# Performance work log

Measured on AMD Instinct MI355X. Metric: run time of the kernel, lower is better.

Reference implementation:

```python
import jax, jax.numpy as jnp
import numpy as np

MARGIN = 0.1
PERM_SEED = 42  # fixed stand-in for torch.randperm per row


def setup_inputs() -> dict:
    key = jax.random.key(0)
    k1, k2, k3 = jax.random.split(key, 3)
    n, d, f = 32768, 1000, 300
    inputs = jax.random.normal(k1, (n, f), dtype=jnp.float32)
    Y = jax.random.normal(k2, (d, f), dtype=jnp.float32)
    y_idxs = jax.random.randint(k3, (n,), 0, d)
    return {"inputs": inputs, "Y": Y, "y_idxs": y_idxs}


def reference(inputs, Y, y_idxs):
    # inputs: [n, f], Y: [d, f] class semantic embeddings, y_idxs: [n]
    n, d = inputs.shape[0], Y.shape[0]

    # All dot products at once: S[i, j] = Y[j] . inputs[i]
    S = inputs @ Y.T  # [n, d]

    # One random class permutation per row (torch.randperm(d) per sample)
    perm_keys = jax.random.split(jax.random.key(PERM_SEED), n)
    perms = jax.vmap(lambda k: jax.random.permutation(k, d))(perm_keys)  # [n, d]

    ap = S[jnp.arange(n), y_idxs]                 # [n]   anchor-positive dots
    an = jnp.take_along_axis(S, perms, axis=1)    # [n, d] anchor-negative dots in perm order

    valid = perms != y_idxs[:, None]              # skip j == y
    # early-break condition at each permutation slot
    cond = valid & ((ap[:, None] - an) > MARGIN)
    c = cond.astype(jnp.int32)
    excl_cum = jnp.cumsum(c, axis=1) - c          # exclusive cumsum of break events
    # include every valid slot up to AND including the first breaking slot
    include = valid & (excl_cum == 0)             # [n, d]

    # MarginRankingLoss with target=1: mean(max(0, margin + an - ap))
    per_pair = jnp.maximum(0.0, MARGIN + an - ap[:, None])
    total = jnp.sum(jnp.where(include, per_pair, 0.0))
    count = jnp.maximum(jnp.sum(include), 1).astype(jnp.float32)
    return total / count
```

## Files before the change

### kernel.cpp

```cpp
#include <hip/hip_runtime.h>
#include <stdint.h>

#define N_ROWS 32768
#define D_CLS  1000
#define D_PAD  1024
#define F_DIM  300
#define F_PAD  320
#define MARGIN 0.1f

#define BM     128
#define BN     128
#define BK     64
#define GTHR   512
#define LDTA   328
#define LDTB   72

#define M_PB   32
#define NTHR   512
#define NT_PW  8
#define MT_PB  2
#define LDA    328
#define SROW   34

#define NPART  32

typedef short short8 __attribute__((ext_vector_type(8)));
typedef float f32x4  __attribute__((ext_vector_type(4)));

__device__ __forceinline__ uint32_t rotl32(uint32_t x, int r) {
  return (x << r) | (x >> (32 - r));
}

__device__ __forceinline__ void threefry2x32(uint32_t k0, uint32_t k1,
                                             uint32_t x0, uint32_t x1,
                                             uint32_t& o0, uint32_t& o1) {
  uint32_t k2 = k0 ^ k1 ^ 0x1BD11BDAu;
  x0 += k0; x1 += k1;
#define TF_R(r) { x0 += x1; x1 = rotl32(x1, (r)); x1 ^= x0; }
  TF_R(13) TF_R(15) TF_R(26) TF_R(6)
  x0 += k1; x1 += k2 + 1u;
  TF_R(17) TF_R(29) TF_R(16) TF_R(24)
  x0 += k2; x1 += k0 + 2u;
  TF_R(13) TF_R(15) TF_R(26) TF_R(6)
  x0 += k0; x1 += k1 + 3u;
  TF_R(17) TF_R(29) TF_R(16) TF_R(24)
  x0 += k1; x1 += k2 + 4u;
  TF_R(13) TF_R(15) TF_R(26) TF_R(6)
  x0 += k2; x1 += k0 + 5u;
#undef TF_R
  o0 = x0; o1 = x1;
}

struct TFSched {
  uint32_t k0, k1, k2, k2p1, k0p2, k1p3, k2p4, k0p5;
};
__device__ __forceinline__ TFSched tf_make(uint32_t k0, uint32_t k1) {
  TFSched s;
  s.k0 = k0; s.k1 = k1;
  s.k2 = k0 ^ k1 ^ 0x1BD11BDAu;
  s.k2p1 = s.k2 + 1u; s.k0p2 = k0 + 2u; s.k1p3 = k1 + 3u;
  s.k2p4 = s.k2 + 4u; s.k0p5 = k0 + 5u;
  return s;
}
__device__ __forceinline__ uint32_t tf_hash(const TFSched& s, uint32_t c) {
  uint32_t x0 = s.k0, x1 = c + s.k1;
#define TFH(r) { x0 += x1; x1 = __builtin_amdgcn_alignbit(x1, x1, 32 - (r)); x1 ^= x0; }
  TFH(13) TFH(15) TFH(26) TFH(6)
  x0 += s.k1; x1 += s.k2p1;
  TFH(17) TFH(29) TFH(16) TFH(24)
  x0 += s.k2; x1 += s.k0p2;
  TFH(13) TFH(15) TFH(26) TFH(6)
  x0 += s.k0; x1 += s.k1p3;
  TFH(17) TFH(29) TFH(16) TFH(24)
  x0 += s.k1; x1 += s.k2p4;
  TFH(13) TFH(15) TFH(26) TFH(6)
  x0 += s.k2; x1 += s.k0p5;
#undef TFH
  return x0 ^ x1;
}

__device__ __forceinline__ uint16_t f2bf(float f) {
  uint32_t u = __builtin_bit_cast(uint32_t, f);
  return (uint16_t)((u + 0x7FFFu + ((u >> 16) & 1u)) >> 16);
}
__device__ __forceinline__ float bf2f(uint16_t v) {
  return __builtin_bit_cast(float, (uint32_t)v << 16);
}
__device__ __forceinline__ float bf2f_lo(uint32_t v) {
  return __builtin_bit_cast(float, v << 16);
}
__device__ __forceinline__ float bf2f_hi(uint32_t v) {
  return __builtin_bit_cast(float, v & 0xFFFF0000u);
}

__global__ void prep(const float* __restrict__ Y, uint16_t* __restrict__ Ybf,
                     uint32_t* __restrict__ subk) {
  int i = blockIdx.x * 256 + threadIdx.x;
  if (i < D_PAD * F_PAD) {
    int j = i / F_PAD;
    int k = i - j * F_PAD;
    float v = (j < D_CLS && k < F_DIM) ? Y[j * F_DIM + k] : 0.f;
    Ybf[i] = f2bf(v);
  }
  if (i < N_ROWS) {
    uint32_t r1, r2, s1, s2;
    threefry2x32(0u, 42u, 0u, (uint32_t)i, r1, r2);
    threefry2x32(r1, r2, 0u, 1u, s1, s2);
    subk[2 * i]     = s1;
    subk[2 * i + 1] = s2;
  }
}

__launch_bounds__(GTHR, 1)
__global__ void gemm_s(const float* __restrict__ inputs,
                       const uint16_t* __restrict__ Ybf,
                       uint32_t* __restrict__ Spair) {
  __shared__ __align__(16) uint16_t A_lds[BM * LDTA];
  __shared__ __align__(16) uint16_t B_lds[2][BN * LDTB];

  const int t    = threadIdx.x;
  const int wave = t >> 6;
  const int lane = t & 63;
  const int l15  = lane & 15;
  const int g    = lane >> 4;
  const int wm   = wave >> 1;
  const int wn   = wave & 1;
  const int r0   = blockIdx.x * BM;

  for (int i = t; i < BM * (F_DIM / 4); i += GTHR) {
    int r  = i / 75;
    int c4 = i - r * 75;
    float4 v = *(const float4*)(inputs + (size_t)(r0 + r) * F_DIM + c4 * 4);
    ushort4 o;
    o.x = f2bf(v.x); o.y = f2bf(v.y); o.z = f2bf(v.z); o.w = f2bf(v.w);
    *(ushort4*)&A_lds[r * LDTA + c4 * 4] = o;
  }
  for (int i = t; i < BM * 7; i += GTHR) {
    int r = i / 7, p = i - r * 7;
    *(ushort4*)&A_lds[r * LDTA + 300 + p * 4] = (ushort4){0, 0, 0, 0};
  }

  const int brow = t >> 3, bkof = t & 7;
  short8 bv[2];
  auto LOADB = [&](int tile) {
    const int c0 = (tile / 5) * BN;
    const int k0 = (tile % 5) * BK;
#pragma unroll
    for (int j = 0; j < 2; ++j)
      bv[j] = *(const short8*)(Ybf + (size_t)(c0 + j * 64 + brow) * F_PAD + k0 + bkof * 8);
  };
  auto WRITEB = [&](int buf) {
#pragma unroll
    for (int j = 0; j < 2; ++j)
      *(short8*)&B_lds[buf][(j * 64 + brow) * LDTB + bkof * 8] = bv[j];
  };

  f32x4 acc[2][4];
#pragma unroll
  for (int mt = 0; mt < 2; ++mt)
#pragma unroll
    for (int nt = 0; nt < 4; ++nt) acc[mt][nt] = (f32x4){0.f, 0.f, 0.f, 0.f};

  LOADB(0);
  __syncthreads();
  WRITEB(0);
  __syncthreads();

  const int NT = 8 * 5;
#pragma unroll 1
  for (int tile = 0; tile < NT; ++tile) {
    const int kt = tile % 5;
    if (tile < NT - 1) LOADB(tile + 1);
    const uint16_t* Bc = B_lds[tile & 1];
#pragma unroll
    for (int ks = 0; ks < 2; ++ks) {
      short8 a[2], b[4];
#pragma unroll
      for (int mt = 0; mt < 2; ++mt)
        a[mt] = *(const short8*)&A_lds[(wm * 32 + mt * 16 + l15) * LDTA + kt * BK + ks * 32 + g * 8];
#pragma unroll
      for (int nt = 0; nt < 4; ++nt)
        b[nt] = *(const short8*)&Bc[(wn * 64 + nt * 16 + l15) * LDTB + ks * 32 + g * 8];
#pragma unroll
      for (int mt = 0; mt < 2; ++mt)
#pragma unroll
        for (int nt = 0; nt < 4; ++nt)
          acc[mt][nt] = __builtin_amdgcn_mfma_f32_16x16x32_bf16(a[mt], b[nt], acc[mt][nt], 0, 0, 0);
    }
    if (kt == 4) {
      const int c0 = (tile / 5) * BN;
#pragma unroll
      for (int mt = 0; mt < 2; ++mt)
#pragma unroll
        for (int nt = 0; nt < 4; ++nt) {
          const int col = c0 + wn * 64 + nt * 16 + l15;
#pragma unroll
          for (int p = 0; p < 2; ++p) {
            uint32_t lo = f2bf(acc[mt][nt][2 * p]);
            uint32_t hi = f2bf(acc[mt][nt][2 * p + 1]);
            size_t rp = (size_t)(r0 >> 1) + wm * 16 + mt * 8 + g * 2 + p;
            Spair[rp * D_PAD + col] = (hi << 16) | lo;
          }
          acc[mt][nt] = (f32x4){0.f, 0.f, 0.f, 0.f};
        }
    }
    if (tile < NT - 1) {
      WRITEB((tile + 1) & 1);
      __syncthreads();
    }
  }
}

__launch_bounds__(256, 2)
__global__ void hash_loss(const uint32_t* __restrict__ Spair,
                          const uint32_t* __restrict__ subk,
                          const int* __restrict__ yidx,
                          float* __restrict__ rowSum,
                          int* __restrict__ rowCnt) {
  const int lane = threadIdx.x & 63;
  const int wave = threadIdx.x >> 6;
  const int rp   = blockIdx.x * 4 + wave;
  const int rA   = 2 * rp;
  const int rB   = 2 * rp + 1;

  const int yA = yidx[rA], yB = yidx[rB];
  const TFSched sA = tf_make(subk[2 * rA], subk[2 * rA + 1]);
  const TFSched sB = tf_make(subk[2 * rB], subk[2 * rB + 1]);

  const uint32_t* Sp = Spair + (size_t)rp * D_PAD;
  const float apA = bf2f_lo(Sp[yA]);
  const float apB = bf2f_hi(Sp[yB]);

  uint32_t an[16];
#pragma unroll
  for (int j = 0; j < 4; ++j) {
    uint4 v = *(const uint4*)(Sp + j * 256 + lane * 4);
    an[4 * j + 0] = v.x; an[4 * j + 1] = v.y;
    an[4 * j + 2] = v.z; an[4 * j + 3] = v.w;
  }

  uint32_t skAB[16];
  uint32_t pkA = 0xFFFFFFFFu, pkB = 0xFFFFFFFFu;
#pragma unroll
  for (int q = 0; q < 16; ++q) {
    const int c = (q >> 2) * 256 + lane * 4 + (q & 3);
    uint32_t kA = tf_hash(sA, (uint32_t)c);
    uint32_t kB = tf_hash(sB, (uint32_t)c);
    skAB[q] = (kA >> 16) | (kB & 0xFFFF0000u);
    float anA = bf2f_lo(an[q]);
    float anB = bf2f_hi(an[q]);
    if ((c < D_CLS) && (c != yA) && (apA - anA) > MARGIN) {
      pkA = (kA < pkA) ? kA : pkA;
    }
    if ((c < D_CLS) && (c != yB) && (apB - anB) > MARGIN) {
      pkB = (kB < pkB) ? kB : pkB;
    }
  }
#pragma unroll
  for (int off = 1; off < 64; off <<= 1) {
    uint32_t oA = __shfl_xor(pkA, off, 64);
    uint32_t oB = __shfl_xor(pkB, off, 64);
    pkA = (oA < pkA) ? oA : pkA;
    pkB = (oB < pkB) ? oB : pkB;
  }
  const uint32_t pA16 = pkA >> 16;
  const uint32_t pB16 = pkB >> 16;

  float smA = 0.f, smB = 0.f; int ctA = 0, ctB = 0;
#pragma unroll
  for (int q = 0; q < 16; ++q) {
    const int c = (q >> 2) * 256 + lane * 4 + (q & 3);
    float anA = bf2f_lo(an[q]);
    float anB = bf2f_hi(an[q]);
    if ((c < D_CLS) && (c != yA) && (skAB[q] & 0xFFFFu) < pA16) {
      smA += MARGIN + anA - apA; ctA += 1;
    }
    if ((c < D_CLS) && (c != yB) && (skAB[q] >> 16) < pB16) {
      smB += MARGIN + anB - apB; ctB += 1;
    }
  }
#pragma unroll
  for (int off = 1; off < 64; off <<= 1) {
    smA += __shfl_xor(smA, off, 64);
    smB += __shfl_xor(smB, off, 64);
    ctA += __shfl_xor(ctA, off, 64);
    ctB += __shfl_xor(ctB, off, 64);
  }
  if (lane == 0) {
    rowSum[rA] = smA;
    rowCnt[rA] = ctA + (pkA != 0xFFFFFFFFu ? 1 : 0);
    rowSum[rB] = smB;
    rowCnt[rB] = ctB + (pkB != 0xFFFFFFFFu ? 1 : 0);
  }
}

__launch_bounds__(NTHR, 4)
__global__ void triplet_fused(const float* __restrict__ inputs,
                              const uint16_t* __restrict__ Ybf,
                              const int* __restrict__ yidx,
                              float* __restrict__ rowSum,
                              int* __restrict__ rowCnt) {
  __shared__ __align__(16) uint16_t SH[D_PAD * SROW];
  __shared__ int      y_sh[M_PB];
  __shared__ uint32_t subk_sh[M_PB][2];

  const int t    = threadIdx.x;
  const int wave = t >> 6;
  const int lane = t & 63;
  const int l15  = lane & 15;
  const int g    = lane >> 4;
  const int row0 = blockIdx.x * M_PB;
  const int colbase = wave * (NT_PW * 16);

  if (t < M_PB) {
    y_sh[t] = yidx[row0 + t];
    uint32_t r1, r2, s1, s2;
    threefry2x32(0u, 42u, 0u, (uint32_t)(row0 + t), r1, r2);
    threefry2x32(r1, r2, 0u, 1u, s1, s2);
    subk_sh[t][0] = s1; subk_sh[t][1] = s2;
  }

  uint16_t* A_fl = SH;
  for (int i = t; i < M_PB * (F_DIM / 4); i += NTHR) {
    int r  = i / 75;
    int c4 = i - r * 75;
    float4 v = *(const float4*)(inputs + (size_t)(row0 + r) * F_DIM + c4 * 4);
    ushort4 o;
    o.x = f2bf(v.x); o.y = f2bf(v.y); o.z = f2bf(v.z); o.w = f2bf(v.w);
    *(ushort4*)&A_fl[r * LDA + c4 * 4] = o;
  }
  for (int i = t; i < M_PB * 5; i += NTHR) {
    int r = i / 5, p = i - r * 5;
    *(ushort4*)&A_fl[r * LDA + 300 + p * 4] = (ushort4){0, 0, 0, 0};
  }
  __syncthreads();

  f32x4 acc[MT_PB][NT_PW];
#pragma unroll
  for (int mt = 0; mt < MT_PB; ++mt)
#pragma unroll
    for (int nt = 0; nt < NT_PW; ++nt) acc[mt][nt] = (f32x4){0.f, 0.f, 0.f, 0.f};

  const uint16_t* gB[NT_PW];
#pragma unroll
  for (int nt = 0; nt < NT_PW; ++nt) {
    int j = colbase + nt * 16 + l15;
    gB[nt] = Ybf + (size_t)j * F_PAD + (g << 3);
  }
  const uint16_t* aBase = &A_fl[l15 * LDA + (g << 3)];

#pragma unroll 2
  for (int ks = 0; ks < F_PAD / 32; ++ks) {
    short8 b[NT_PW], a[MT_PB];
#pragma unroll
    for (int nt = 0; nt < NT_PW; ++nt)
      b[nt] = *(const short8*)(gB[nt] + ks * 32);
#pragma unroll
    for (int mt = 0; mt < MT_PB; ++mt)
      a[mt] = *(const short8*)(aBase + mt * 16 * LDA + ks * 32);
#pragma unroll
    for (int mt = 0; mt < MT_PB; ++mt)
#pragma unroll
      for (int nt = 0; nt < NT_PW; ++nt)
        acc[mt][nt] = __builtin_amdgcn_mfma_f32_16x16x32_bf16(a[mt], b[nt], acc[mt][nt], 0, 0, 0);
  }

  __syncthreads();

#pragma unroll
  for (int mt = 0; mt < MT_PB; ++mt)
#pragma unroll
    for (int nt = 0; nt < NT_PW; ++nt) {
      int col = colbase + nt * 16 + l15;
#pragma unroll
      for (int p = 0; p < 2; ++p) {
        uint32_t lo = f2bf(acc[mt][nt][2 * p]);
        uint32_t hi = f2bf(acc[mt][nt][2 * p + 1]);
        *(uint32_t*)&SH[col * SROW + mt * 16 + (g << 2) + 2 * p] = (hi << 16) | lo;
      }
    }
  __syncthreads();

#pragma unroll
  for (int pr = 0; pr < 2; ++pr) {
    const int rA = wave * 4 + pr * 2;
    const int rB = rA + 1;
    const int yA = y_sh[rA], yB = y_sh[rB];
    const uint32_t a1 = subk_sh[rA][0], a2 = subk_sh[rA][1];
    const uint32_t b1 = subk_sh[rB][0], b2 = subk_sh[rB][1];
    const float apA = bf2f(SH[yA * SROW + rA]);
    const float apB = bf2f(SH[yB * SROW + rB]);

    uint32_t skA[16], skB[16];
    uint32_t pkA = 0xFFFFFFFFu, pkB = 0xFFFFFFFFu;
#pragma unroll
    for (int q = 0; q < 16; ++q) {
      const int c = q * 64 + lane;
      uint32_t xA, yAo, xB, yBo;
      threefry2x32(a1, a2, 0u, (uint32_t)c, xA, yAo);
      threefry2x32(b1, b2, 0u, (uint32_t)c, xB, yBo);
      skA[q] = xA ^ yAo;
      skB[q] = xB ^ yBo;
      float anA = bf2f(SH[c * SROW + rA]);
      float anB = bf2f(SH[c * SROW + rB]);
      if ((c < D_CLS) && (c != yA) && (apA - anA) > MARGIN) {
        pkA = (skA[q] < pkA) ? skA[q] : pkA;
      }
      if ((c < D_CLS) && (c != yB) && (apB - anB) > MARGIN) {
        pkB = (skB[q] < pkB) ? skB[q] : pkB;
      }
    }
#pragma unroll
    for (int off = 1; off < 64; off <<= 1) {
      uint32_t oA = __shfl_xor(pkA, off, 64);
      uint32_t oB = __shfl_xor(pkB, off, 64);
      pkA = (oA < pkA) ? oA : pkA;
      pkB = (oB < pkB) ? oB : pkB;
    }
    float smA = 0.f, smB = 0.f; int ctA = 0, ctB = 0;
#pragma unroll
    for (int q = 0; q < 16; ++q) {
      const int c = q * 64 + lane;
      float anA = bf2f(SH[c * SROW + rA]);
      float anB = bf2f(SH[c * SROW + rB]);
      if ((c < D_CLS) && (c != yA) && skA[q] < pkA) { smA += MARGIN + anA - apA; ctA += 1; }
      if ((c < D_CLS) && (c != yB) && skB[q] < pkB) { smB += MARGIN + anB - apB; ctB += 1; }
    }
#pragma unroll
    for (int off = 1; off < 64; off <<= 1) {
      smA += __shfl_xor(smA, off, 64);
      smB += __shfl_xor(smB, off, 64);
      ctA += __shfl_xor(ctA, off, 64);
      ctB += __shfl_xor(ctB, off, 64);
    }
    if (lane == 0) {
      rowSum[row0 + rA] = smA;
      rowCnt[row0 + rA] = ctA + (pkA != 0xFFFFFFFFu ? 1 : 0);
      rowSum[row0 + rB] = smB;
      rowCnt[row0 + rB] = ctB + (pkB != 0xFFFFFFFFu ? 1 : 0);
    }
  }
}

__global__ void reduce_part(const float* __restrict__ rowSum,
                            const int* __restrict__ rowCnt,
                            float* __restrict__ pS, int* __restrict__ pC) {
  __shared__ float ss[4];
  __shared__ int   sc[4];
  const int base = blockIdx.x * (N_ROWS / NPART);
  float s = 0.f; int c = 0;
  for (int i = threadIdx.x; i < N_ROWS / NPART; i += 256) {
    s += rowSum[base + i];
    c += rowCnt[base + i];
  }
#pragma unroll
  for (int off = 32; off > 0; off >>= 1) {
    s += __shfl_down(s, (unsigned)off, 64);
    c += __shfl_down(c, (unsigned)off, 64);
  }
  int wid = threadIdx.x >> 6, lane = threadIdx.x & 63;
  if (lane == 0) { ss[wid] = s; sc[wid] = c; }
  __syncthreads();
  if (threadIdx.x == 0) {
    pS[blockIdx.x] = ss[0] + ss[1] + ss[2] + ss[3];
    pC[blockIdx.x] = sc[0] + sc[1] + sc[2] + sc[3];
  }
}

__global__ void reduce_final(const float* __restrict__ pS,
                             const int* __restrict__ pC,
                             float* __restrict__ out) {
  const int lane = threadIdx.x;
  float s = (lane < NPART) ? pS[lane] : 0.f;
  int   c = (lane < NPART) ? pC[lane] : 0;
#pragma unroll
  for (int off = 32; off > 0; off >>= 1) {
    s += __shfl_down(s, (unsigned)off, 64);
    c += __shfl_down(c, (unsigned)off, 64);
  }
  if (lane == 0) out[0] = s / (float)(c < 1 ? 1 : c);
}

extern "C" void kernel_launch(void* const* d_in, const int* in_sizes, int n_in,
                              void* d_out, int out_size, void* d_ws, size_t ws_size,
                              hipStream_t stream) {
  const float* inputs = (const float*)d_in[0];
  const float* Y      = (const float*)d_in[1];
  const int*   yidx   = (const int*)d_in[2];
  float* out = (float*)d_out;

  char* ws = (char*)d_ws;
  size_t off = 0;
  uint16_t* Ybf    = (uint16_t*)(ws + off); off += (size_t)D_PAD * F_PAD * 2;
  float*    rowSum = (float*)(ws + off);    off += (size_t)N_ROWS * 4;
  int*      rowCnt = (int*)(ws + off);      off += (size_t)N_ROWS * 4;
  uint32_t* subk   = (uint32_t*)(ws + off); off += (size_t)N_ROWS * 8;
  float*    pS     = (float*)(ws + off);    off += (size_t)NPART * 4;
  int*      pC     = (int*)(ws + off);      off += (size_t)NPART * 4;
  off = (off + 255) & ~(size_t)255;
  uint32_t* Spair  = (uint32_t*)(ws + off); off += (size_t)(N_ROWS / 2) * D_PAD * 4;
  const size_t need = off;

  hipLaunchKernelGGL(prep, dim3((D_PAD * F_PAD + 255) / 256), dim3(256),
                     0, stream, Y, Ybf, subk);
  if (ws_size >= need) {
    hipLaunchKernelGGL(gemm_s, dim3(N_ROWS / BM), dim3(GTHR),
                       0, stream, inputs, Ybf, Spair);
    hipLaunchKernelGGL(hash_loss, dim3(N_ROWS / 8), dim3(256),
                       0, stream, Spair, subk, yidx, rowSum, rowCnt);
  } else {
    hipLaunchKernelGGL(triplet_fused, dim3(N_ROWS / M_PB), dim3(NTHR),
                       0, stream, inputs, Ybf, yidx, rowSum, rowCnt);
  }
  hipLaunchKernelGGL(reduce_part, dim3(NPART), dim3(256), 0, stream,
                     rowSum, rowCnt, pS, pC);
  hipLaunchKernelGGL(reduce_final, dim3(1), dim3(64), 0, stream, pS, pC, out);
}
```

Before: 122.6 us.

## Fuse permutation hashing and loss epilogue into the GEMM kernel

Turns the GEMM into a template that, in fused mode, computes threefry permutation keys for its block's rows between MFMA tiles, writes them to a new keyP buffer, and runs the per-row min-key/loss reduction after the GEMM loop. This removes the separate hash_loss launch and is meant to hide the hash ALU work under the matrix compute. In exchange it needs an extra workspace buffer of the same size as Spair, plus extra global traffic to write and reread keys. The path is taken only when the workspace is large enough; otherwise it falls back to the old two-kernel path. The epilogue reads Spair written by other waves in the block after only a __syncthreads, which relies on global write visibility within the block.

```diff
diff --git a/kernel.cpp b/kernel.cpp
--- a/kernel.cpp
+++ b/kernel.cpp
@@ -111,10 +111,16 @@
   }
 }
 
+template<int FUSED>
 __launch_bounds__(GTHR, 1)
-__global__ void gemm_s(const float* __restrict__ inputs,
-                       const uint16_t* __restrict__ Ybf,
-                       uint32_t* __restrict__ Spair) {
+__global__ void gemm_core(const float* __restrict__ inputs,
+                          const uint16_t* __restrict__ Ybf,
+                          uint32_t* __restrict__ Spair,
+                          uint32_t* __restrict__ keyP,
+                          const uint32_t* __restrict__ subk,
+                          const int* __restrict__ yidx,
+                          float* __restrict__ rowSum,
+                          int* __restrict__ rowCnt) {
   __shared__ __align__(16) uint16_t A_lds[BM * LDTA];
   __shared__ __align__(16) uint16_t B_lds[2][BN * LDTB];
 
@@ -171,6 +177,25 @@
   for (int tile = 0; tile < NT; ++tile) {
     const int kt = tile % 5;
     if (tile < NT - 1) LOADB(tile + 1);
+
+    if (FUSED && tile < 32) {
+#pragma unroll
+      for (int mm = 0; mm < 2; ++mm) {
+        const int m = 2 * tile + mm;
+        const size_t rpg = (size_t)(r0 >> 1) + m;
+        const int rA = r0 + 2 * m;
+        const TFSched sA = tf_make(subk[2 * rA],     subk[2 * rA + 1]);
+        const TFSched sB = tf_make(subk[2 * rA + 2], subk[2 * rA + 3]);
+#pragma unroll
+        for (int half = 0; half < 2; ++half) {
+          const uint32_t c = (uint32_t)(t + 512 * half);
+          uint32_t kA = tf_hash(sA, c);
+          uint32_t kB = tf_hash(sB, c);
+          keyP[rpg * D_PAD + c] = (kA >> 16) | (kB & 0xFFFF0000u);
+        }
+      }
+    }
+
     const uint16_t* Bc = B_lds[tile & 1];
 #pragma unroll
     for (int ks = 0; ks < 2; ++ks) {
@@ -207,6 +232,70 @@
     if (tile < NT - 1) {
       WRITEB((tile + 1) & 1);
       __syncthreads();
+    }
+  }
+
+  if (FUSED) {
+    __syncthreads();
+#pragma unroll 1
+    for (int j = 0; j < 8; ++j) {
+      const int rp_loc = wave * 8 + j;
+      const size_t rpg = (size_t)(r0 >> 1) + rp_loc;
+      const int rA = r0 + 2 * rp_loc;
+      const int yA = yidx[rA], yB = yidx[rA + 1];
+      const uint32_t* Sp = Spair + rpg * D_PAD;
+      const uint32_t* Kp = keyP  + rpg * D_PAD;
+      const float apA = bf2f_lo(Sp[yA]);
+      const float apB = bf2f_hi(Sp[yB]);
+
+      uint32_t an[16], kk[16];
+#pragma unroll
+      for (int q4 = 0; q4 < 4; ++q4) {
+        uint4 v = *(const uint4*)(Sp + q4 * 256 + lane * 4);
+        an[4 * q4 + 0] = v.x; an[4 * q4 + 1] = v.y;
+        an[4 * q4 + 2] = v.z; an[4 * q4 + 3] = v.w;
+        uint4 w = *(const uint4*)(Kp + q4 * 256 + lane * 4);
+        kk[4 * q4 + 0] = w.x; kk[4 * q4 + 1] = w.y;
+        kk[4 * q4 + 2] = w.z; kk[4 * q4 + 3] = w.w;
+      }
+
+      uint32_t mnA = 0xFFFFu, mnB = 0xFFFFu;
+#pragma unroll
+      for (int q = 0; q < 16; ++q) {
+        const int c = (q >> 2) * 256 + lane * 4 + (q & 3);
+        const uint32_t kA = kk[q] & 0xFFFFu, kB = kk[q] >> 16;
+        const float anA = bf2f_lo(an[q]), anB = bf2f_hi(an[q]);
+        if ((c < D_CLS) && (c != yA) && (apA - anA) > MARGIN) mnA = (kA < mnA) ? kA : mnA;
+        if ((c < D_CLS) && (c != yB) && (apB - anB) > MARGIN) mnB = (kB < mnB) ? kB : mnB;
+      }
+#pragma unroll
+      for (int off = 1; off < 64; off <<= 1) {
+        uint32_t oA = __shfl_xor(mnA, off, 64);
+        uint32_t oB = __shfl_xor(mnB, off, 64);
+        mnA = (oA < mnA) ? oA : mnA;
+        mnB = (oB < mnB) ? oB : mnB;
+      }
+
+      float smA = 0.f, smB = 0.f; int ctA = 0, ctB = 0;
+#pragma unroll
+      for (int q = 0; q < 16; ++q) {
+        const int c = (q >> 2) * 256 + lane * 4 + (q & 3);
+        const uint32_t kA = kk[q] & 0xFFFFu, kB = kk[q] >> 16;
+        const float anA = bf2f_lo(an[q]), anB = bf2f_hi(an[q]);
+        if ((c < D_CLS) && (c != yA) && kA < mnA) { smA += MARGIN + anA - apA; ctA += 1; }
+        if ((c < D_CLS) && (c != yB) && kB < mnB) { smB += MARGIN + anB - apB; ctB += 1; }
+      }
+#pragma unroll
+      for (int off = 1; off < 64; off <<= 1) {
+        smA += __shfl_xor(smA, off, 64);
+        smB += __shfl_xor(smB, off, 64);
+        ctA += __shfl_xor(ctA, off, 64);
+        ctB += __shfl_xor(ctB, off, 64);
+      }
+      if (lane == 0) {
+        rowSum[rA]     = smA;  rowCnt[rA]     = ctA + (mnA != 0xFFFFu ? 1 : 0);
+        rowSum[rA + 1] = smB;  rowCnt[rA + 1] = ctB + (mnB != 0xFFFFu ? 1 : 0);
+      }
     }
   }
 }
@@ -499,13 +588,19 @@
   int*      pC     = (int*)(ws + off);      off += (size_t)NPART * 4;
   off = (off + 255) & ~(size_t)255;
   uint32_t* Spair  = (uint32_t*)(ws + off); off += (size_t)(N_ROWS / 2) * D_PAD * 4;
-  const size_t need = off;
+  const size_t need_mid = off;
+  off = (off + 255) & ~(size_t)255;
+  uint32_t* keyP   = (uint32_t*)(ws + off); off += (size_t)(N_ROWS / 2) * D_PAD * 4;
+  const size_t need_full = off;
 
   hipLaunchKernelGGL(prep, dim3((D_PAD * F_PAD + 255) / 256), dim3(256),
                      0, stream, Y, Ybf, subk);
-  if (ws_size >= need) {
-    hipLaunchKernelGGL(gemm_s, dim3(N_ROWS / BM), dim3(GTHR),
-                       0, stream, inputs, Ybf, Spair);
+  if (ws_size >= need_full) {
+    gemm_core<1><<<dim3(N_ROWS / BM), dim3(GTHR), 0, stream>>>(
+        inputs, Ybf, Spair, keyP, subk, yidx, rowSum, rowCnt);
+  } else if (ws_size >= need_mid) {
+    gemm_core<0><<<dim3(N_ROWS / BM), dim3(GTHR), 0, stream>>>(
+        inputs, Ybf, Spair, (uint32_t*)nullptr, subk, yidx, rowSum, rowCnt);
     hipLaunchKernelGGL(hash_loss, dim3(N_ROWS / 8), dim3(256),
                        0, stream, Spair, subk, yidx, rowSum, rowCnt);
   } else {
```

Measured after the change: 138.0 us. 12.6% more time.

## Drop split GEMM+hash path, use fused kernel with precomputed threefry schedule

Applied to the files above, without the earlier changes.

Removes the two-kernel path that materialized a bf16 score matrix in global memory and then ran a separate hash/loss pass. The fused per-block kernel now always runs, and its hash loop uses the precomputed threefry key schedule (tf_make/tf_hash) and 16-bit packed sort keys instead of full threefry calls with 32-bit keys. This avoids a large global write and re-read of scores. The cost is the fused kernel's own GEMM tiling and LDS use. The 16-bit key truncation carries a small risk of ties changing which slots are included.

```diff
diff --git a/kernel.cpp b/kernel.cpp
--- a/kernel.cpp
+++ b/kernel.cpp
@@ -7,13 +7,6 @@
 #define F_DIM  300
 #define F_PAD  320
 #define MARGIN 0.1f
-
-#define BM     128
-#define BN     128
-#define BK     64
-#define GTHR   512
-#define LDTA   328
-#define LDTB   72
 
 #define M_PB   32
 #define NTHR   512
@@ -86,211 +79,14 @@
 __device__ __forceinline__ float bf2f(uint16_t v) {
   return __builtin_bit_cast(float, (uint32_t)v << 16);
 }
-__device__ __forceinline__ float bf2f_lo(uint32_t v) {
-  return __builtin_bit_cast(float, v << 16);
-}
-__device__ __forceinline__ float bf2f_hi(uint32_t v) {
-  return __builtin_bit_cast(float, v & 0xFFFF0000u);
-}
-
-__global__ void prep(const float* __restrict__ Y, uint16_t* __restrict__ Ybf,
-                     uint32_t* __restrict__ subk) {
+
+__global__ void prep(const float* __restrict__ Y, uint16_t* __restrict__ Ybf) {
   int i = blockIdx.x * 256 + threadIdx.x;
   if (i < D_PAD * F_PAD) {
     int j = i / F_PAD;
     int k = i - j * F_PAD;
     float v = (j < D_CLS && k < F_DIM) ? Y[j * F_DIM + k] : 0.f;
     Ybf[i] = f2bf(v);
-  }
-  if (i < N_ROWS) {
-    uint32_t r1, r2, s1, s2;
-    threefry2x32(0u, 42u, 0u, (uint32_t)i, r1, r2);
-    threefry2x32(r1, r2, 0u, 1u, s1, s2);
-    subk[2 * i]     = s1;
-    subk[2 * i + 1] = s2;
-  }
-}
-
-__launch_bounds__(GTHR, 1)
-__global__ void gemm_s(const float* __restrict__ inputs,
-                       const uint16_t* __restrict__ Ybf,
-                       uint32_t* __restrict__ Spair) {
-  __shared__ __align__(16) uint16_t A_lds[BM * LDTA];
-  __shared__ __align__(16) uint16_t B_lds[2][BN * LDTB];
-
-  const int t    = threadIdx.x;
-  const int wave = t >> 6;
-  const int lane = t & 63;
-  const int l15  = lane & 15;
-  const int g    = lane >> 4;
-  const int wm   = wave >> 1;
-  const int wn   = wave & 1;
-  const int r0   = blockIdx.x * BM;
-
-  for (int i = t; i < BM * (F_DIM / 4); i += GTHR) {
-    int r  = i / 75;
-    int c4 = i - r * 75;
-    float4 v = *(const float4*)(inputs + (size_t)(r0 + r) * F_DIM + c4 * 4);
-    ushort4 o;
-    o.x = f2bf(v.x); o.y = f2bf(v.y); o.z = f2bf(v.z); o.w = f2bf(v.w);
-    *(ushort4*)&A_lds[r * LDTA + c4 * 4] = o;
-  }
-  for (int i = t; i < BM * 7; i += GTHR) {
-    int r = i / 7, p = i - r * 7;
-    *(ushort4*)&A_lds[r * LDTA + 300 + p * 4] = (ushort4){0, 0, 0, 0};
-  }
-
-  const int brow = t >> 3, bkof = t & 7;
-  short8 bv[2];
-  auto LOADB = [&](int tile) {
-    const int c0 = (tile / 5) * BN;
-    const int k0 = (tile % 5) * BK;
-#pragma unroll
-    for (int j = 0; j < 2; ++j)
-      bv[j] = *(const short8*)(Ybf + (size_t)(c0 + j * 64 + brow) * F_PAD + k0 + bkof * 8);
-  };
-  auto WRITEB = [&](int buf) {
-#pragma unroll
-    for (int j = 0; j < 2; ++j)
-      *(short8*)&B_lds[buf][(j * 64 + brow) * LDTB + bkof * 8] = bv[j];
-  };
-
-  f32x4 acc[2][4];
-#pragma unroll
-  for (int mt = 0; mt < 2; ++mt)
-#pragma unroll
-    for (int nt = 0; nt < 4; ++nt) acc[mt][nt] = (f32x4){0.f, 0.f, 0.f, 0.f};
-
-  LOADB(0);
-  __syncthreads();
-  WRITEB(0);
-  __syncthreads();
-
-  const int NT = 8 * 5;
-#pragma unroll 1
-  for (int tile = 0; tile < NT; ++tile) {
-    const int kt = tile % 5;
-    if (tile < NT - 1) LOADB(tile + 1);
-    const uint16_t* Bc = B_lds[tile & 1];
-#pragma unroll
-    for (int ks = 0; ks < 2; ++ks) {
-      short8 a[2], b[4];
-#pragma unroll
-      for (int mt = 0; mt < 2; ++mt)
-        a[mt] = *(const short8*)&A_lds[(wm * 32 + mt * 16 + l15) * LDTA + kt * BK + ks * 32 + g * 8];
-#pragma unroll
-      for (int nt = 0; nt < 4; ++nt)
-        b[nt] = *(const short8*)&Bc[(wn * 64 + nt * 16 + l15) * LDTB + ks * 32 + g * 8];
-#pragma unroll
-      for (int mt = 0; mt < 2; ++mt)
-#pragma unroll
-        for (int nt = 0; nt < 4; ++nt)
-          acc[mt][nt] = __builtin_amdgcn_mfma_f32_16x16x32_bf16(a[mt], b[nt], acc[mt][nt], 0, 0, 0);
-    }
-    if (kt == 4) {
-      const int c0 = (tile / 5) * BN;
-#pragma unroll
-      for (int mt = 0; mt < 2; ++mt)
-#pragma unroll
-        for (int nt = 0; nt < 4; ++nt) {
-          const int col = c0 + wn * 64 + nt * 16 + l15;
-#pragma unroll
-          for (int p = 0; p < 2; ++p) {
-            uint32_t lo = f2bf(acc[mt][nt][2 * p]);
-            uint32_t hi = f2bf(acc[mt][nt][2 * p + 1]);
-            size_t rp = (size_t)(r0 >> 1) + wm * 16 + mt * 8 + g * 2 + p;
-            Spair[rp * D_PAD + col] = (hi << 16) | lo;
-          }
-          acc[mt][nt] = (f32x4){0.f, 0.f, 0.f, 0.f};
-        }
-    }
-    if (tile < NT - 1) {
-      WRITEB((tile + 1) & 1);
-      __syncthreads();
-    }
-  }
-}
-
-__launch_bounds__(256, 2)
-__global__ void hash_loss(const uint32_t* __restrict__ Spair,
-                          const uint32_t* __restrict__ subk,
-                          const int* __restrict__ yidx,
-                          float* __restrict__ rowSum,
-                          int* __restrict__ rowCnt) {
-  const int lane = threadIdx.x & 63;
-  const int wave = threadIdx.x >> 6;
-  const int rp   = blockIdx.x * 4 + wave;
-  const int rA   = 2 * rp;
-  const int rB   = 2 * rp + 1;
-
-  const int yA = yidx[rA], yB = yidx[rB];
-  const TFSched sA = tf_make(subk[2 * rA], subk[2 * rA + 1]);
-  const TFSched sB = tf_make(subk[2 * rB], subk[2 * rB + 1]);
-
-  const uint32_t* Sp = Spair + (size_t)rp * D_PAD;
-  const float apA = bf2f_lo(Sp[yA]);
-  const float apB = bf2f_hi(Sp[yB]);
-
-  uint32_t an[16];
-#pragma unroll
-  for (int j = 0; j < 4; ++j) {
-    uint4 v = *(const uint4*)(Sp + j * 256 + lane * 4);
-    an[4 * j + 0] = v.x; an[4 * j + 1] = v.y;
-    an[4 * j + 2] = v.z; an[4 * j + 3] = v.w;
-  }
-
-  uint32_t skAB[16];
-  uint32_t pkA = 0xFFFFFFFFu, pkB = 0xFFFFFFFFu;
-#pragma unroll
-  for (int q = 0; q < 16; ++q) {
-    const int c = (q >> 2) * 256 + lane * 4 + (q & 3);
-    uint32_t kA = tf_hash(sA, (uint32_t)c);
-    uint32_t kB = tf_hash(sB, (uint32_t)c);
-    skAB[q] = (kA >> 16) | (kB & 0xFFFF0000u);
-    float anA = bf2f_lo(an[q]);
-    float anB = bf2f_hi(an[q]);
-    if ((c < D_CLS) && (c != yA) && (apA - anA) > MARGIN) {
-      pkA = (kA < pkA) ? kA : pkA;
-    }
-    if ((c < D_CLS) && (c != yB) && (apB - anB) > MARGIN) {
-      pkB = (kB < pkB) ? kB : pkB;
-    }
-  }
-#pragma unroll
-  for (int off = 1; off < 64; off <<= 1) {
-    uint32_t oA = __shfl_xor(pkA, off, 64);
-    uint32_t oB = __shfl_xor(pkB, off, 64);
-    pkA = (oA < pkA) ? oA : pkA;
-    pkB = (oB < pkB) ? oB : pkB;
-  }
-  const uint32_t pA16 = pkA >> 16;
-  const uint32_t pB16 = pkB >> 16;
-
-  float smA = 0.f, smB = 0.f; int ctA = 0, ctB = 0;
-#pragma unroll
-  for (int q = 0; q < 16; ++q) {
-    const int c = (q >> 2) * 256 + lane * 4 + (q & 3);
-    float anA = bf2f_lo(an[q]);
-    float anB = bf2f_hi(an[q]);
-    if ((c < D_CLS) && (c != yA) && (skAB[q] & 0xFFFFu) < pA16) {
-      smA += MARGIN + anA - apA; ctA += 1;
-    }
-    if ((c < D_CLS) && (c != yB) && (skAB[q] >> 16) < pB16) {
-      smB += MARGIN + anB - apB; ctB += 1;
-    }
-  }
-#pragma unroll
-  for (int off = 1; off < 64; off <<= 1) {
-    smA += __shfl_xor(smA, off, 64);
-    smB += __shfl_xor(smB, off, 64);
-    ctA += __shfl_xor(ctA, off, 64);
-    ctB += __shfl_xor(ctB, off, 64);
-  }
-  if (lane == 0) {
-    rowSum[rA] = smA;
-    rowCnt[rA] = ctA + (pkA != 0xFFFFFFFFu ? 1 : 0);
-    rowSum[rB] = smB;
-    rowCnt[rB] = ctB + (pkB != 0xFFFFFFFFu ? 1 : 0);
   }
 }
 
@@ -381,33 +177,31 @@
     }
   __syncthreads();
 
-#pragma unroll
+#pragma unroll 1
   for (int pr = 0; pr < 2; ++pr) {
     const int rA = wave * 4 + pr * 2;
     const int rB = rA + 1;
     const int yA = y_sh[rA], yB = y_sh[rB];
-    const uint32_t a1 = subk_sh[rA][0], a2 = subk_sh[rA][1];
-    const uint32_t b1 = subk_sh[rB][0], b2 = subk_sh[rB][1];
+    const TFSched sA = tf_make(subk_sh[rA][0], subk_sh[rA][1]);
+    const TFSched sB = tf_make(subk_sh[rB][0], subk_sh[rB][1]);
     const float apA = bf2f(SH[yA * SROW + rA]);
     const float apB = bf2f(SH[yB * SROW + rB]);
 
-    uint32_t skA[16], skB[16];
+    uint32_t skAB[16];
     uint32_t pkA = 0xFFFFFFFFu, pkB = 0xFFFFFFFFu;
 #pragma unroll
     for (int q = 0; q < 16; ++q) {
       const int c = q * 64 + lane;
-      uint32_t xA, yAo, xB, yBo;
-      threefry2x32(a1, a2, 0u, (uint32_t)c, xA, yAo);
-      threefry2x32(b1, b2, 0u, (uint32_t)c, xB, yBo);
-      skA[q] = xA ^ yAo;
-      skB[q] = xB ^ yBo;
+      uint32_t kA = tf_hash(sA, (uint32_t)c);
+      uint32_t kB = tf_hash(sB, (uint32_t)c);
+      skAB[q] = (kA >> 16) | (kB & 0xFFFF0000u);
       float anA = bf2f(SH[c * SROW + rA]);
       float anB = bf2f(SH[c * SROW + rB]);
       if ((c < D_CLS) && (c != yA) && (apA - anA) > MARGIN) {
-        pkA = (skA[q] < pkA) ? skA[q] : pkA;
+        pkA = (kA < pkA) ? kA : pkA;
       }
       if ((c < D_CLS) && (c != yB) && (apB - anB) > MARGIN) {
-        pkB = (skB[q] < pkB) ? skB[q] : pkB;
+        pkB = (kB < pkB) ? kB : pkB;
       }
     }
 #pragma unroll
@@ -417,14 +211,21 @@
       pkA = (oA < pkA) ? oA : pkA;
       pkB = (oB < pkB) ? oB : pkB;
     }
+    const uint32_t pA16 = pkA >> 16;
+    const uint32_t pB16 = pkB >> 16;
+
     float smA = 0.f, smB = 0.f; int ctA = 0, ctB = 0;
 #pragma unroll
     for (int q = 0; q < 16; ++q) {
       const int c = q * 64 + lane;
       float anA = bf2f(SH[c * SROW + rA]);
       float anB = bf2f(SH[c * SROW + rB]);
-      if ((c < D_CLS) && (c != yA) && skA[q] < pkA) { smA += MARGIN + anA - apA; ctA += 1; }
-      if ((c < D_CLS) && (c != yB) && skB[q] < pkB) { smB += MARGIN + anB - apB; ctB += 1; }
+      if ((c < D_CLS) && (c != yA) && (skAB[q] & 0xFFFFu) < pA16) {
+        smA += MARGIN + anA - apA; ctA += 1;
+      }
+      if ((c < D_CLS) && (c != yB) && (skAB[q] >> 16) < pB16) {
+        smB += MARGIN + anB - apB; ctB += 1;
+      }
     }
 #pragma unroll
     for (int off = 1; off < 64; off <<= 1) {
@@ -494,24 +295,13 @@
   uint16_t* Ybf    = (uint16_t*)(ws + off); off += (size_t)D_PAD * F_PAD * 2;
   float*    rowSum = (float*)(ws + off);    off += (size_t)N_ROWS * 4;
   int*      rowCnt = (int*)(ws + off);      off += (size_t)N_ROWS * 4;
-  uint32_t* subk   = (uint32_t*)(ws + off); off += (size_t)N_ROWS * 8;
   float*    pS     = (float*)(ws + off);    off += (size_t)NPART * 4;
   int*      pC     = (int*)(ws + off);      off += (size_t)NPART * 4;
-  off = (off + 255) & ~(size_t)255;
-  uint32_t* Spair  = (uint32_t*)(ws + off); off += (size_t)(N_ROWS / 2) * D_PAD * 4;
-  const size_t need = off;
 
   hipLaunchKernelGGL(prep, dim3((D_PAD * F_PAD + 255) / 256), dim3(256),
-                     0, stream, Y, Ybf, subk);
-  if (ws_size >= need) {
-    hipLaunchKernelGGL(gemm_s, dim3(N_ROWS / BM), dim3(GTHR),
-                       0, stream, inputs, Ybf, Spair);
-    hipLaunchKernelGGL(hash_loss, dim3(N_ROWS / 8), dim3(256),
-                       0, stream, Spair, subk, yidx, rowSum, rowCnt);
-  } else {
-    hipLaunchKernelGGL(triplet_fused, dim3(N_ROWS / M_PB), dim3(NTHR),
-                       0, stream, inputs, Ybf, yidx, rowSum, rowCnt);
-  }
+                     0, stream, Y, Ybf);
+  hipLaunchKernelGGL(triplet_fused, dim3(N_ROWS / M_PB), dim3(NTHR),
+                     0, stream, inputs, Ybf, yidx, rowSum, rowCnt);
   hipLaunchKernelGGL(reduce_part, dim3(NPART), dim3(256), 0, stream,
                      rowSum, rowCnt, pS, pC);
   hipLaunchKernelGGL(reduce_final, dim3(1), dim3(64), 0, stream, pS, pC, out);
```

After: 151.6 us. +23.6%, slower.
